# Performance work log

Measured on AMD Instinct MI355X. Metric: run time of the kernel, lower is better.

The kernel has to match this reference:

```python
import jax, jax.numpy as jnp
import numpy as np

POOLING_SIZE = 7          # cfg.POOLING_SIZE
SPATIAL_SCALE = 1.0 / 16.0  # feat_stride 16


def setup_inputs() -> dict:
    key = jax.random.key(0)
    k1, k2 = jax.random.split(key)
    C, H, W = 512, 38, 63  # VGG16 conv5_3 feature map, stride 16
    N = 1024               # number of proposals
    bottom = jax.random.normal(k1, (1, C, H, W), dtype=jnp.float32)
    # build rois in image-pixel coords: [batch_idx, x1, y1, x2, y2]
    Himg, Wimg = H * 16.0, W * 16.0
    u = jax.random.uniform(k2, (N, 4), dtype=jnp.float32)
    x1 = u[:, 0] * (Wimg - 48.0)
    y1 = u[:, 1] * (Himg - 48.0)
    x2 = x1 + 16.0 + u[:, 2] * (Wimg - 1.0 - 16.0 - x1)
    y2 = y1 + 16.0 + u[:, 3] * (Himg - 1.0 - 16.0 - y1)
    rois = jnp.stack([jnp.zeros((N,), jnp.float32), x1, y1, x2, y2], axis=1)
    return {"bottom": bottom, "rois": rois}


def _crop_and_resize(image, boxes, box_ind, crop):
    # image: [B,C,H,W]; boxes: [N,4] normalized (y1,x1,y2,x2) wrt (H-1),(W-1)
    B, C, H, W = image.shape
    y1, x1, y2, x2 = boxes[:, 0], boxes[:, 1], boxes[:, 2], boxes[:, 3]
    t = jnp.arange(crop, dtype=image.dtype) / (crop - 1)          # [crop]
    in_y = (y1[:, None] + t[None, :] * (y2 - y1)[:, None]) * (H - 1)  # [N,crop]
    in_x = (x1[:, None] + t[None, :] * (x2 - x1)[:, None]) * (W - 1)  # [N,crop]
    valid = (((in_y >= 0) & (in_y <= H - 1))[:, :, None]
             & ((in_x >= 0) & (in_x <= W - 1))[:, None, :])       # [N,ch,cw]
    y0f = jnp.floor(in_y)
    x0f = jnp.floor(in_x)
    wy = (in_y - y0f)[:, :, None, None]  # lerp frac, broadcast over cw,C
    wx = (in_x - x0f)[:, None, :, None]
    y0 = jnp.clip(y0f, 0, H - 1).astype(jnp.int32)
    y1i = jnp.clip(y0f + 1, 0, H - 1).astype(jnp.int32)
    x0 = jnp.clip(x0f, 0, W - 1).astype(jnp.int32)
    x1i = jnp.clip(x0f + 1, 0, W - 1).astype(jnp.int32)
    b = box_ind[:, None, None]
    # advanced-index gathers -> [N, ch, cw, C]
    g00 = image[b, :, y0[:, :, None], x0[:, None, :]]
    g01 = image[b, :, y0[:, :, None], x1i[:, None, :]]
    g10 = image[b, :, y1i[:, :, None], x0[:, None, :]]
    g11 = image[b, :, y1i[:, :, None], x1i[:, None, :]]
    top = g00 + (g01 - g00) * wx
    bot = g10 + (g11 - g10) * wx
    val = top + (bot - top) * wy
    val = jnp.where(valid[:, :, :, None], val, 0.0)  # extrapolation_value = 0
    return jnp.transpose(val, (0, 3, 1, 2))  # [N, C, ch, cw]


def reference(bottom, rois):
    # faithful translation of Network._crop_pool_layer(bottom, rois, max_pool=True)
    B, C, H, W = bottom.shape
    x1 = rois[:, 1] * SPATIAL_SCALE
    y1 = rois[:, 2] * SPATIAL_SCALE
    x2 = rois[:, 3] * SPATIAL_SCALE
    y2 = rois[:, 4] * SPATIAL_SCALE
    boxes = jnp.stack([y1 / (H - 1), x1 / (W - 1),
                       y2 / (H - 1), x2 / (W - 1)], axis=1)
    box_ind = rois[:, 0].astype(jnp.int32)
    pre = POOLING_SIZE * 2  # 14
    crops = _crop_and_resize(bottom, boxes, box_ind, pre)  # [N,C,14,14]
    N = crops.shape[0]
    # max_pool2d(2,2) -> [N,C,7,7]
    pooled = crops.reshape(N, C, POOLING_SIZE, 2, POOLING_SIZE, 2).max(axis=(3, 5))
    return pooled
```

## Files before the change

### kernel.cpp

```cpp
#include <hip/hip_runtime.h>
#include <math.h>

#define CC 512
#define HH 38
#define WW 63
#define HWSZ (HH * WW)
#define NROIS 1024
#define NP 49
#define CHUNK 132

typedef float   f32x4 __attribute__((ext_vector_type(4)));
typedef _Float16 f16x8 __attribute__((ext_vector_type(8)));
typedef _Float16 f16x2 __attribute__((ext_vector_type(2)));

__global__ __launch_bounds__(256) void transpose_cvt(
        const float* __restrict__ src, _Float16* __restrict__ dst) {
    __shared__ float tile[64][65];
    int s0 = blockIdx.x * 64;
    int c0 = blockIdx.y * 64;
    int tx = threadIdx.x & 63;
    int ty = threadIdx.x >> 6;

#pragma unroll
    for (int k = 0; k < 16; ++k) {
        int c = ty * 16 + k;
        int s = s0 + tx;
        float v = (s < HWSZ) ? src[(c0 + c) * HWSZ + s] : 0.0f;
        tile[tx][c] = v;
    }
    __syncthreads();

    int u = threadIdx.x & 31;
    int vv = threadIdx.x >> 5;
#pragma unroll
    for (int k = 0; k < 8; ++k) {
        int s = vv * 8 + k;
        if (s0 + s < HWSZ) {
            f16x2 h;
            h[0] = (_Float16)tile[s][2 * u];
            h[1] = (_Float16)tile[s][2 * u + 1];
            *(f16x2*)(dst + (size_t)(s0 + s) * CC + c0 + 2 * u) = h;
        }
    }
}

__global__ __launch_bounds__(256) void roi_pool_v10(
        const _Float16* __restrict__ img,
        const float* __restrict__ rois,
        float* __restrict__ out) {
    __shared__ float stage[14 * 7 * CHUNK];

    int n = blockIdx.x >> 2;
    int q = blockIdx.x & 3;
    int t = threadIdx.x;
    int g = t & 15;
    int slot = t >> 4;

    const float* r = rois + n * 5;
    float x1n = (r[1] * 0.0625f) / 62.0f;
    float y1n = (r[2] * 0.0625f) / 37.0f;
    float x2n = (r[3] * 0.0625f) / 62.0f;
    float y2n = (r[4] * 0.0625f) / 37.0f;
    float ydn = y2n - y1n;
    float xdn = x2n - x1n;

    if (slot < 14) {
        int iy = slot;
        float tty = (float)iy * (1.0f / 13.0f);
        float in_y = (y1n + tty * ydn) * 37.0f;
        bool vy = (in_y >= 0.0f) && (in_y <= 37.0f);
        float y0f = floorf(in_y);
        float wy = in_y - y0f;
        int yb0 = (int)fminf(fmaxf(y0f, 0.0f), 37.0f) * (WW * CC);
        int yb1 = (int)fminf(fmaxf(y0f + 1.0f, 0.0f), 37.0f) * (WW * CC);

        const _Float16* imgc = img + (q << 7) + (g << 3);

        float acc[8];
#pragma unroll
        for (int j = 0; j < 8; ++j) acc[j] = -INFINITY;

#pragma unroll
        for (int ix = 0; ix < 14; ++ix) {
            float ttx = (float)ix * (1.0f / 13.0f);
            float in_x = (x1n + ttx * xdn) * 62.0f;
            bool vx = (in_x >= 0.0f) && (in_x <= 62.0f);
            float x0f = floorf(in_x);
            float wx = in_x - x0f;
            int xo0 = (int)fminf(fmaxf(x0f, 0.0f), 62.0f) << 9;
            int xo1 = (int)fminf(fmaxf(x0f + 1.0f, 0.0f), 62.0f) << 9;

            f16x8 g00 = *(const f16x8*)(imgc + yb0 + xo0);
            f16x8 g01 = *(const f16x8*)(imgc + yb0 + xo1);
            f16x8 g10 = *(const f16x8*)(imgc + yb1 + xo0);
            f16x8 g11 = *(const f16x8*)(imgc + yb1 + xo1);

            _Float16 wxh = (_Float16)wx;
            f16x8 toph = g00 + (g01 - g00) * wxh;
            f16x8 both = g10 + (g11 - g10) * wxh;

            bool valid = vx && vy;
#pragma unroll
            for (int j = 0; j < 8; ++j) {
                float tf = (float)toph[j];
                float bf = (float)both[j];
                float val = tf + (bf - tf) * wy;
                val = valid ? val : 0.0f;
                acc[j] = fmaxf(acc[j], val);
            }

            if (ix & 1) {
                int ox = ix >> 1;
                int base = (iy * 7 + ox) * CHUNK + (g << 3);
                f32x4 a, b;
#pragma unroll
                for (int j = 0; j < 4; ++j) { a[j] = acc[j]; b[j] = acc[j + 4]; }
                *(f32x4*)(stage + base)     = a;
                *(f32x4*)(stage + base + 4) = b;
#pragma unroll
                for (int j = 0; j < 8; ++j) acc[j] = -INFINITY;
            }
        }
    }

    __syncthreads();

    f32x4* o4 = (f32x4*)(out + ((n << 9) + (q << 7)) * NP);
    for (int i = t; i < (128 * NP) / 4; i += 256) {
        int m = i << 2;
        f32x4 v;
#pragma unroll
        for (int j = 0; j < 4; ++j) {
            int mm = m + j;
            int c  = mm / 49;
            int p  = mm - c * 49;
            int oy = p / 7;
            int ox = p - oy * 7;
            int base = (14 * oy + ox) * CHUNK + c;
            v[j] = fmaxf(stage[base], stage[base + 7 * CHUNK]);
        }
        __builtin_nontemporal_store(v, &o4[i]);
    }
}

__global__ __launch_bounds__(256) void roi_pool_chw(
        const float* __restrict__ img,
        const float* __restrict__ rois,
        float* __restrict__ out) {
    __shared__ float stage[256 * NP];
    int n = blockIdx.x >> 1;
    int h = blockIdx.x & 1;
    int t = threadIdx.x;
    int c = (h << 8) + t;

    const float* r = rois + n * 5;
    float x1n = (r[1] * 0.0625f) / 62.0f;
    float y1n = (r[2] * 0.0625f) / 37.0f;
    float x2n = (r[3] * 0.0625f) / 62.0f;
    float y2n = (r[4] * 0.0625f) / 37.0f;
    float ydn = y2n - y1n;
    float xdn = x2n - x1n;

    const float* imgc = img + c * HWSZ;

    float wxa[14];
    int   x0a[14], x1a[14];
    int   vxm = 0;
#pragma unroll
    for (int ix = 0; ix < 14; ++ix) {
        float tt = (float)ix * (1.0f / 13.0f);
        float in_x = (x1n + tt * xdn) * 62.0f;
        if (in_x >= 0.0f && in_x <= 62.0f) vxm |= (1 << ix);
        float x0f = floorf(in_x);
        wxa[ix] = in_x - x0f;
        x0a[ix] = (int)fminf(fmaxf(x0f, 0.0f), 62.0f);
        x1a[ix] = (int)fminf(fmaxf(x0f + 1.0f, 0.0f), 62.0f);
    }

#pragma unroll
    for (int oy = 0; oy < 7; ++oy) {
        float row[7];
#pragma unroll
        for (int ox = 0; ox < 7; ++ox) row[ox] = -INFINITY;
#pragma unroll
        for (int sy = 0; sy < 2; ++sy) {
            int iy = oy * 2 + sy;
            float tt = (float)iy * (1.0f / 13.0f);
            float in_y = (y1n + tt * ydn) * 37.0f;
            bool vy = (in_y >= 0.0f) && (in_y <= 37.0f);
            float y0f = floorf(in_y);
            float wy = in_y - y0f;
            int yy0 = (int)fminf(fmaxf(y0f, 0.0f), 37.0f);
            int yy1 = (int)fminf(fmaxf(y0f + 1.0f, 0.0f), 37.0f);
            int yb0 = yy0 * WW;
            int yb1 = yy1 * WW;
#pragma unroll
            for (int ox = 0; ox < 7; ++ox) {
#pragma unroll
                for (int sx = 0; sx < 2; ++sx) {
                    int ix = ox * 2 + sx;
                    float g00 = imgc[yb0 + x0a[ix]];
                    float g01 = imgc[yb0 + x1a[ix]];
                    float g10 = imgc[yb1 + x0a[ix]];
                    float g11 = imgc[yb1 + x1a[ix]];
                    float wx = wxa[ix];
                    float top = g00 + (g01 - g00) * wx;
                    float bot = g10 + (g11 - g10) * wx;
                    float val = top + (bot - top) * wy;
                    bool valid = vy && ((vxm >> ix) & 1);
                    val = valid ? val : 0.0f;
                    row[ox] = fmaxf(row[ox], val);
                }
            }
        }
#pragma unroll
        for (int ox = 0; ox < 7; ++ox)
            stage[t * NP + oy * 7 + ox] = row[ox];
    }

    __syncthreads();
    const float4* s4 = (const float4*)stage;
    float4* o4 = (float4*)(out + ((n << 9) + (h << 8)) * NP);
    for (int i = t; i < (256 * NP) / 4; i += 256)
        o4[i] = s4[i];
}

extern "C" void kernel_launch(void* const* d_in, const int* in_sizes, int n_in,
                              void* d_out, int out_size, void* d_ws, size_t ws_size,
                              hipStream_t stream) {
    const float* bottom = (const float*)d_in[0];
    const float* rois   = (const float*)d_in[1];
    float* out = (float*)d_out;

    const size_t need = (size_t)CC * HWSZ * sizeof(_Float16);
    if (ws_size >= need) {
        _Float16* img = (_Float16*)d_ws;
        dim3 tg((HWSZ + 63) / 64, CC / 64);
        transpose_cvt<<<tg, 256, 0, stream>>>(bottom, img);
        roi_pool_v10<<<NROIS * 4, 256, 0, stream>>>(img, rois, out);
    } else {
        roi_pool_chw<<<NROIS * 2, 256, 0, stream>>>(bottom, rois, out);
    }
}
```

Before: 162.7 us.

## Reduce vertical pool pairs via warp shuffle and stage outputs in final layout

The vertical 2x max is now taken in registers with a cross-lane shuffle between adjacent row slots. Only even-row lanes write to shared memory, and they write directly in the output [c][49] layout, so the epilogue becomes a plain vectorized copy with no div/mod index math. Bilinear gathers are also skipped for invalid sample points, which are folded in as a max with zero. The cost is scattered, possibly bank-conflicting shared stores (stride 49) and some divergent branching in exchange.

```diff
diff --git a/kernel.cpp b/kernel.cpp
--- a/kernel.cpp
+++ b/kernel.cpp
@@ -7,9 +7,8 @@
 #define HWSZ (HH * WW)
 #define NROIS 1024
 #define NP 49
-#define CHUNK 132
-
-typedef float   f32x4 __attribute__((ext_vector_type(4)));
+
+typedef float    f32x4 __attribute__((ext_vector_type(4)));
 typedef _Float16 f16x8 __attribute__((ext_vector_type(8)));
 typedef _Float16 f16x2 __attribute__((ext_vector_type(2)));
 
@@ -44,11 +43,11 @@
     }
 }
 
-__global__ __launch_bounds__(256) void roi_pool_v10(
+__global__ __launch_bounds__(256) void roi_pool_v11(
         const _Float16* __restrict__ img,
         const float* __restrict__ rois,
         float* __restrict__ out) {
-    __shared__ float stage[14 * 7 * CHUNK];
+    __shared__ float stage[128 * NP];
 
     int n = blockIdx.x >> 2;
     int q = blockIdx.x & 3;
@@ -66,6 +65,7 @@
 
     if (slot < 14) {
         int iy = slot;
+        int oy = iy >> 1;
         float tty = (float)iy * (1.0f / 13.0f);
         float in_y = (y1n + tty * ydn) * 37.0f;
         bool vy = (in_y >= 0.0f) && (in_y <= 37.0f);
@@ -76,71 +76,70 @@
 
         const _Float16* imgc = img + (q << 7) + (g << 3);
 
-        float acc[8];
-#pragma unroll
-        for (int j = 0; j < 8; ++j) acc[j] = -INFINITY;
-
-#pragma unroll
-        for (int ix = 0; ix < 14; ++ix) {
-            float ttx = (float)ix * (1.0f / 13.0f);
-            float in_x = (x1n + ttx * xdn) * 62.0f;
-            bool vx = (in_x >= 0.0f) && (in_x <= 62.0f);
-            float x0f = floorf(in_x);
-            float wx = in_x - x0f;
-            int xo0 = (int)fminf(fmaxf(x0f, 0.0f), 62.0f) << 9;
-            int xo1 = (int)fminf(fmaxf(x0f + 1.0f, 0.0f), 62.0f) << 9;
-
-            f16x8 g00 = *(const f16x8*)(imgc + yb0 + xo0);
-            f16x8 g01 = *(const f16x8*)(imgc + yb0 + xo1);
-            f16x8 g10 = *(const f16x8*)(imgc + yb1 + xo0);
-            f16x8 g11 = *(const f16x8*)(imgc + yb1 + xo1);
-
-            _Float16 wxh = (_Float16)wx;
-            f16x8 toph = g00 + (g01 - g00) * wxh;
-            f16x8 both = g10 + (g11 - g10) * wxh;
-
-            bool valid = vx && vy;
+#pragma unroll
+        for (int ox = 0; ox < 7; ++ox) {
+            float acc[8];
+#pragma unroll
+            for (int j = 0; j < 8; ++j) acc[j] = -INFINITY;
+            bool inv = false;
+
+#pragma unroll
+            for (int sx = 0; sx < 2; ++sx) {
+                int ix = ox * 2 + sx;
+                float ttx = (float)ix * (1.0f / 13.0f);
+                float in_x = (x1n + ttx * xdn) * 62.0f;
+                bool vx = (in_x >= 0.0f) && (in_x <= 62.0f);
+                float x0f = floorf(in_x);
+                float wx = in_x - x0f;
+                int xo0 = (int)fminf(fmaxf(x0f, 0.0f), 62.0f) << 9;
+                int xo1 = (int)fminf(fmaxf(x0f + 1.0f, 0.0f), 62.0f) << 9;
+
+                bool valid = vx && vy;
+                if (valid) {
+                    f16x8 g00 = *(const f16x8*)(imgc + yb0 + xo0);
+                    f16x8 g01 = *(const f16x8*)(imgc + yb0 + xo1);
+                    f16x8 g10 = *(const f16x8*)(imgc + yb1 + xo0);
+                    f16x8 g11 = *(const f16x8*)(imgc + yb1 + xo1);
+
+                    _Float16 wxh = (_Float16)wx;
+                    f16x8 toph = g00 + (g01 - g00) * wxh;
+                    f16x8 both = g10 + (g11 - g10) * wxh;
+
+#pragma unroll
+                    for (int j = 0; j < 8; ++j) {
+                        float tf = (float)toph[j];
+                        float bf = (float)both[j];
+                        acc[j] = fmaxf(acc[j], tf + (bf - tf) * wy);
+                    }
+                } else {
+                    inv = true;
+                }
+            }
+            if (inv) {
+#pragma unroll
+                for (int j = 0; j < 8; ++j) acc[j] = fmaxf(acc[j], 0.0f);
+            }
+
 #pragma unroll
             for (int j = 0; j < 8; ++j) {
-                float tf = (float)toph[j];
-                float bf = (float)both[j];
-                float val = tf + (bf - tf) * wy;
-                val = valid ? val : 0.0f;
-                acc[j] = fmaxf(acc[j], val);
-            }
-
-            if (ix & 1) {
-                int ox = ix >> 1;
-                int base = (iy * 7 + ox) * CHUNK + (g << 3);
-                f32x4 a, b;
-#pragma unroll
-                for (int j = 0; j < 4; ++j) { a[j] = acc[j]; b[j] = acc[j + 4]; }
-                *(f32x4*)(stage + base)     = a;
-                *(f32x4*)(stage + base + 4) = b;
-#pragma unroll
-                for (int j = 0; j < 8; ++j) acc[j] = -INFINITY;
+                float o = __shfl_xor(acc[j], 16);
+                acc[j] = fmaxf(acc[j], o);
+            }
+            if (!(slot & 1)) {
+                int pos = oy * 7 + ox;
+#pragma unroll
+                for (int j = 0; j < 8; ++j)
+                    stage[(g * 8 + j) * NP + pos] = acc[j];
             }
         }
     }
 
     __syncthreads();
 
+    const f32x4* s4 = (const f32x4*)stage;
     f32x4* o4 = (f32x4*)(out + ((n << 9) + (q << 7)) * NP);
-    for (int i = t; i < (128 * NP) / 4; i += 256) {
-        int m = i << 2;
-        f32x4 v;
-#pragma unroll
-        for (int j = 0; j < 4; ++j) {
-            int mm = m + j;
-            int c  = mm / 49;
-            int p  = mm - c * 49;
-            int oy = p / 7;
-            int ox = p - oy * 7;
-            int base = (14 * oy + ox) * CHUNK + c;
-            v[j] = fmaxf(stage[base], stage[base + 7 * CHUNK]);
-        }
-        __builtin_nontemporal_store(v, &o4[i]);
-    }
+    for (int i = t; i < (128 * NP) / 4; i += 256)
+        __builtin_nontemporal_store(s4[i], &o4[i]);
 }
 
 __global__ __launch_bounds__(256) void roi_pool_chw(
@@ -237,7 +236,7 @@
         _Float16* img = (_Float16*)d_ws;
         dim3 tg((HWSZ + 63) / 64, CC / 64);
         transpose_cvt<<<tg, 256, 0, stream>>>(bottom, img);
-        roi_pool_v10<<<NROIS * 4, 256, 0, stream>>>(img, rois, out);
+        roi_pool_v11<<<NROIS * 4, 256, 0, stream>>>(img, rois, out);
     } else {
         roi_pool_chw<<<NROIS * 2, 256, 0, stream>>>(bottom, rois, out);
     }
```

After: 153.2 us. 1.06x faster.
